# Performance work log

Hardware: AMD Instinct MI355X
Metric: run time of the kernel (lower is better)

The kernel has to match this reference:

```python
import jax, jax.numpy as jnp
import numpy as np

N, OBS, H, M, L = 512, 32, 128, 128, 3


def _w(key, shape, fan_in):
    return jax.random.normal(key, shape, dtype=jnp.float32) / np.sqrt(fan_in)


def setup_inputs() -> dict:
    key = jax.random.key(0)
    ks = iter(jax.random.split(key, 64))
    inp = {}
    inp["obs"] = jax.random.normal(next(ks), (N, OBS), dtype=jnp.float32)
    inp["pos"] = jax.random.uniform(next(ks), (N, 2), dtype=jnp.float32)
    # encoder: obs_dim -> H -> H -> H
    inp["enc_W1"] = _w(next(ks), (H, OBS), OBS); inp["enc_b1"] = jnp.zeros((H,), jnp.float32)
    inp["enc_W2"] = _w(next(ks), (H, H), H);     inp["enc_b2"] = jnp.zeros((H,), jnp.float32)
    inp["enc_W3"] = _w(next(ks), (H, H), H);     inp["enc_b3"] = jnp.zeros((H,), jnp.float32)
    # per-layer message MLPs: (2H+1) -> M -> M -> M, stacked over L layers
    inp["msg_W1"] = _w(next(ks), (L, M, 2 * H + 1), 2 * H + 1); inp["msg_b1"] = jnp.zeros((L, M), jnp.float32)
    inp["msg_W2"] = _w(next(ks), (L, M, M), M);                 inp["msg_b2"] = jnp.zeros((L, M), jnp.float32)
    inp["msg_W3"] = _w(next(ks), (L, M, M), M);                 inp["msg_b3"] = jnp.zeros((L, M), jnp.float32)
    # per-layer update MLPs: (H+M) -> H -> H -> H, stacked over L layers
    inp["upd_W1"] = _w(next(ks), (L, H, H + M), H + M); inp["upd_b1"] = jnp.zeros((L, H), jnp.float32)
    inp["upd_W2"] = _w(next(ks), (L, H, H), H);         inp["upd_b2"] = jnp.zeros((L, H), jnp.float32)
    inp["upd_W3"] = _w(next(ks), (L, H, H), H);         inp["upd_b3"] = jnp.zeros((L, H), jnp.float32)
    return inp


def _mlp3(x, W1, b1, W2, b2, W3, b3):
    h = jax.nn.relu(x @ W1.T + b1)
    h = jax.nn.relu(h @ W2.T + b2)
    return h @ W3.T + b3


def reference(obs, pos, enc_W1, enc_b1, enc_W2, enc_b2, enc_W3, enc_b3,
              msg_W1, msg_b1, msg_W2, msg_b2, msg_W3, msg_b3,
              upd_W1, upd_b1, upd_W2, upd_b2, upd_W3, upd_b3):
    n = obs.shape[0]
    h = enc_W1.shape[0]
    z = _mlp3(obs, enc_W1, enc_b1, enc_W2, enc_b2, enc_W3, enc_b3)  # (N, H)
    # pairwise distances; guard diagonal sqrt(0) for grad safety, then zero it
    diff = pos[:, None, :] - pos[None, :, :]                  # (N, N, 2)
    sq = jnp.sum(diff * diff, axis=-1)                        # (N, N)
    eye = jnp.eye(n, dtype=pos.dtype)
    dist = jnp.sqrt(jnp.where(eye > 0, 1.0, sq)) * (1.0 - eye)
    nondiag = (1.0 - eye)[:, :, None]
    n_layers = msg_W1.shape[0]
    for l in range(n_layers):
        W1 = msg_W1[l]
        Wi, Wj, wd = W1[:, :h], W1[:, h:2 * h], W1[:, 2 * h]  # split concat [z_i, z_j, d]
        A = z @ Wi.T                                          # (N, M) receiver term
        B = z @ Wj.T                                          # (N, M) sender term
        h1 = jax.nn.relu(A[:, None, :] + B[None, :, :] + dist[:, :, None] * wd + msg_b1[l])  # (N, N, M)
        h2 = jax.nn.relu(jnp.einsum('ijm,km->ijk', h1, msg_W2[l]) + msg_b2[l])
        m = jnp.einsum('ijm,km->ijk', h2, msg_W3[l]) + msg_b3[l]
        m = m * nondiag                                       # exclude j == i
        msum = jnp.sum(m, axis=1)                             # (N, M) sum over senders j
        z = _mlp3(jnp.concatenate([z, msum], axis=-1),
                  upd_W1[l], upd_b1[l], upd_W2[l], upd_b2[l], upd_W3[l], upd_b3[l])
    return z
```

## Files before the change

kernel.cpp:

```cpp
#include <hip/hip_runtime.h>

#define NA 512
#define NOBS 32
#define NH 128

typedef const float* fp32p;
typedef __attribute__((ext_vector_type(8))) short bf16x8;
typedef __attribute__((ext_vector_type(4))) float f32x4;

__device__ __forceinline__ short f2bf(float f) {
    union { float f; unsigned u; } v; v.f = f;
    unsigned r = v.u + 0x7fffu + ((v.u >> 16) & 1u);
    return (short)(r >> 16);
}

__device__ __forceinline__ bf16x8 wfrag_f4(const float* p) {
    float4 u = *(const float4*)p;
    float4 v = *(const float4*)(p + 4);
    bf16x8 f;
    f[0] = f2bf(u.x); f[1] = f2bf(u.y); f[2] = f2bf(u.z); f[3] = f2bf(u.w);
    f[4] = f2bf(v.x); f[5] = f2bf(v.y); f[6] = f2bf(v.z); f[7] = f2bf(v.w);
    return f;
}

#define HSTR 136

__global__ __launch_bounds__(512) void enc_ab_kernel(
    fp32p obs, fp32p eW1, fp32p eb1, fp32p eW2, fp32p eb2, fp32p eW3, fp32p eb3,
    fp32p mW1, float* __restrict__ z, float* __restrict__ A, float* __restrict__ B) {
    const int i = blockIdx.x;
    const int t = threadIdx.x;
    const int nn = t >> 2;
    const int ks = t & 3;

    __shared__ float xs0[NOBS];
    __shared__ float part[4 * NH];
    __shared__ float part2[4 * NH];
    __shared__ float hx[NH], hy[NH], zz[NH];

    if (t < NOBS) xs0[t] = obs[(size_t)i * NOBS + t];
    __syncthreads();
    {
        const float* wr = eW1 + (size_t)nn * NOBS + ks * 8;
        const float4 w0 = *(const float4*)wr;
        const float4 w1 = *(const float4*)(wr + 4);
        const float4 x0 = *(const float4*)&xs0[ks * 8];
        const float4 x1 = *(const float4*)&xs0[ks * 8 + 4];
        part[ks * NH + nn] = w0.x * x0.x + w0.y * x0.y + w0.z * x0.z + w0.w * x0.w +
                             w1.x * x1.x + w1.y * x1.y + w1.z * x1.z + w1.w * x1.w;
    }
    __syncthreads();
    if (t < NH)
        hx[t] = fmaxf(eb1[t] + part[t] + part[NH + t] + part[2 * NH + t] + part[3 * NH + t], 0.f);
    __syncthreads();
    {
        const float* wr = eW2 + (size_t)nn * NH + ks * 4;
        float p = 0.f;
        #pragma unroll
        for (int it = 0; it < 8; ++it) {
            const float4 wv = *(const float4*)(wr + it * 16);
            const float4 xv = *(const float4*)&hx[it * 16 + ks * 4];
            p += wv.x * xv.x + wv.y * xv.y + wv.z * xv.z + wv.w * xv.w;
        }
        part[ks * NH + nn] = p;
    }
    __syncthreads();
    if (t < NH)
        hy[t] = fmaxf(eb2[t] + part[t] + part[NH + t] + part[2 * NH + t] + part[3 * NH + t], 0.f);
    __syncthreads();
    {
        const float* wr = eW3 + (size_t)nn * NH + ks * 4;
        float p = 0.f;
        #pragma unroll
        for (int it = 0; it < 8; ++it) {
            const float4 wv = *(const float4*)(wr + it * 16);
            const float4 xv = *(const float4*)&hy[it * 16 + ks * 4];
            p += wv.x * xv.x + wv.y * xv.y + wv.z * xv.z + wv.w * xv.w;
        }
        part[ks * NH + nn] = p;
    }
    __syncthreads();
    if (t < NH) {
        const float v = eb3[t] + part[t] + part[NH + t] + part[2 * NH + t] + part[3 * NH + t];
        z[(size_t)i * NH + t] = v;
        zz[t] = v;
    }
    __syncthreads();
    {
        const float* pr = mW1 + (size_t)nn * 257;
        float pa = 0.f, pb = 0.f;
        #pragma unroll
        for (int it = 0; it < 8; ++it) {
            #pragma unroll
            for (int j = 0; j < 4; ++j) {
                const int k = it * 16 + ks * 4 + j;
                const float x = zz[k];
                pa += x * pr[k];
                pb += x * pr[NH + k];
            }
        }
        part[ks * NH + nn] = pa;
        part2[ks * NH + nn] = pb;
    }
    __syncthreads();
    if (t < NH) {
        A[(size_t)i * NH + t] = part[t] + part[NH + t] + part[2 * NH + t] + part[3 * NH + t];
        B[(size_t)i * NH + t] = part2[t] + part2[NH + t] + part2[2 * NH + t] + part2[3 * NH + t];
    }
}

__global__ __launch_bounds__(512) void msg_upd_kernel(
    const float* __restrict__ A, const float* __restrict__ B,
    fp32p pos, const float* __restrict__ zin,
    fp32p W1l, fp32p b1, fp32p W2, fp32p b2, fp32p W3, fp32p b3,
    fp32p uW1, fp32p ub1, fp32p uW2, fp32p ub2, fp32p uW3, fp32p ub3,
    fp32p msgW1n, int do_ab,
    float* __restrict__ zout, float* __restrict__ An, float* __restrict__ Bn) {
    const int i = blockIdx.x;
    const int t = threadIdx.x;
    const int lane = t & 63;
    const int w = t >> 6;
    const int q = lane >> 4;
    const int c = lane & 15;
    const int ncol = w * 16 + c;

    __shared__ short h1s[128 * HSTR];
    __shared__ short h2s[128 * HSTR];
    __shared__ float distrow[NA];
    __shared__ float amrow[NH];
    __shared__ float wdsr[NH];
    __shared__ float xs2[2 * NH];
    __shared__ float part[4 * NH];
    __shared__ float part2[4 * NH];
    __shared__ float hx[NH], hy[NH], hz[NH];

    if (t < NH) {
        amrow[t] = A[i * NH + t] + b1[t];
        wdsr[t]  = W1l[t * 257 + 256];
        xs2[t] = zin[(size_t)i * NH + t];
    }
    {
        const float2 pi = *(const float2*)&pos[2 * i];
        const float2 pj = *(const float2*)&pos[2 * t];
        const float dx = pi.x - pj.x, dy = pi.y - pj.y;
        const float s = dx * dx + dy * dy;
        distrow[t] = (t == i) ? 0.0f : sqrtf(s);
    }

    bf16x8 w2f[4], w3f[4];
    {
        const float* w2r = W2 + (size_t)ncol * NH + q * 8;
        const float* w3r = W3 + (size_t)ncol * NH + q * 8;
        #pragma unroll
        for (int kb = 0; kb < 4; ++kb) {
            w2f[kb] = wfrag_f4(w2r + kb * 32);
            w3f[kb] = wfrag_f4(w3r + kb * 32);
        }
    }
    const float b2n = b2[ncol];
    const float b3n = b3[ncol];

    const int m2 = lane * 2;
    float psum = 0.0f;

    for (int c4 = 0; c4 < 4; ++c4) {
        const int j0 = c4 * 128;
        __syncthreads();

        {
            const float am0 = amrow[m2],     am1 = amrow[m2 + 1];
            const float wd0 = wdsr[m2],      wd1 = wdsr[m2 + 1];
            #pragma unroll
            for (int rr = 0; rr < 16; ++rr) {
                const int row = rr * 8 + w;
                const int jg  = j0 + row;
                const float2 bv = *(const float2*)&B[(size_t)jg * NH + m2];
                const float d = distrow[jg];
                const float v0 = fmaxf(am0 + bv.x + d * wd0, 0.0f);
                const float v1 = fmaxf(am1 + bv.y + d * wd1, 0.0f);
                const unsigned p = (unsigned)(unsigned short)f2bf(v0) |
                                   ((unsigned)(unsigned short)f2bf(v1) << 16);
                *(unsigned*)&h1s[row * HSTR + m2] = p;
            }
        }
        __syncthreads();

        #pragma unroll
        for (int jt = 0; jt < 8; ++jt) {
            f32x4 acc = {0.f, 0.f, 0.f, 0.f};
            const short* arow = &h1s[(jt * 16 + c) * HSTR + q * 8];
            #pragma unroll
            for (int kb = 0; kb < 4; ++kb) {
                bf16x8 a = *(const bf16x8*)(arow + kb * 32);
                acc = __builtin_amdgcn_mfma_f32_16x16x32_bf16(a, w2f[kb], acc, 0, 0, 0);
            }
            #pragma unroll
            for (int r = 0; r < 4; ++r) {
                const int row = jt * 16 + q * 4 + r;
                h2s[row * HSTR + ncol] = f2bf(fmaxf(acc[r] + b2n, 0.0f));
            }
        }
        __syncthreads();

        #pragma unroll
        for (int jt = 0; jt < 8; ++jt) {
            f32x4 acc = {0.f, 0.f, 0.f, 0.f};
            const short* arow = &h2s[(jt * 16 + c) * HSTR + q * 8];
            #pragma unroll
            for (int kb = 0; kb < 4; ++kb) {
                bf16x8 a = *(const bf16x8*)(arow + kb * 32);
                acc = __builtin_amdgcn_mfma_f32_16x16x32_bf16(a, w3f[kb], acc, 0, 0, 0);
            }
            #pragma unroll
            for (int r = 0; r < 4; ++r) {
                const int jg = j0 + jt * 16 + q * 4 + r;
                if (jg != i) psum += acc[r] + b3n;
            }
        }
    }

    psum += __shfl_xor(psum, 16, 64);
    psum += __shfl_xor(psum, 32, 64);
    if (lane < 16) xs2[NH + ncol] = psum;
    __syncthreads();

    const int nn = t >> 2;
    const int ks = t & 3;
    {
        const float* wr = uW1 + (size_t)nn * 256 + ks * 4;
        float p = 0.f;
        #pragma unroll
        for (int it = 0; it < 16; ++it) {
            const float4 wv = *(const float4*)(wr + it * 16);
            const float4 xv = *(const float4*)&xs2[it * 16 + ks * 4];
            p += wv.x * xv.x + wv.y * xv.y + wv.z * xv.z + wv.w * xv.w;
        }
        part[ks * NH + nn] = p;
    }
    __syncthreads();
    if (t < NH)
        hx[t] = fmaxf(ub1[t] + part[t] + part[NH + t] + part[2 * NH + t] + part[3 * NH + t], 0.f);
    __syncthreads();
    {
        const float* wr = uW2 + (size_t)nn * NH + ks * 4;
        float p = 0.f;
        #pragma unroll
        for (int it = 0; it < 8; ++it) {
            const float4 wv = *(const float4*)(wr + it * 16);
            const float4 xv = *(const float4*)&hx[it * 16 + ks * 4];
            p += wv.x * xv.x + wv.y * xv.y + wv.z * xv.z + wv.w * xv.w;
        }
        part[ks * NH + nn] = p;
    }
    __syncthreads();
    if (t < NH)
        hy[t] = fmaxf(ub2[t] + part[t] + part[NH + t] + part[2 * NH + t] + part[3 * NH + t], 0.f);
    __syncthreads();
    {
        const float* wr = uW3 + (size_t)nn * NH + ks * 4;
        float p = 0.f;
        #pragma unroll
        for (int it = 0; it < 8; ++it) {
            const float4 wv = *(const float4*)(wr + it * 16);
            const float4 xv = *(const float4*)&hy[it * 16 + ks * 4];
            p += wv.x * xv.x + wv.y * xv.y + wv.z * xv.z + wv.w * xv.w;
        }
        part[ks * NH + nn] = p;
    }
    __syncthreads();
    if (t < NH) {
        const float v = ub3[t] + part[t] + part[NH + t] + part[2 * NH + t] + part[3 * NH + t];
        zout[(size_t)i * NH + t] = v;
        hz[t] = v;
    }
    if (!do_ab) return;
    __syncthreads();
    {
        const float* pr = msgW1n + (size_t)nn * 257;
        float pa = 0.f, pb = 0.f;
        #pragma unroll
        for (int it = 0; it < 8; ++it) {
            #pragma unroll
            for (int j = 0; j < 4; ++j) {
                const int k = it * 16 + ks * 4 + j;
                const float x = hz[k];
                pa += x * pr[k];
                pb += x * pr[NH + k];
            }
        }
        part[ks * NH + nn] = pa;
        part2[ks * NH + nn] = pb;
    }
    __syncthreads();
    if (t < NH) {
        An[(size_t)i * NH + t] = part[t] + part[NH + t] + part[2 * NH + t] + part[3 * NH + t];
        Bn[(size_t)i * NH + t] = part2[t] + part2[NH + t] + part2[2 * NH + t] + part2[3 * NH + t];
    }
}

extern "C" void kernel_launch(void* const* d_in, const int* in_sizes, int n_in,
                              void* d_out, int out_size, void* d_ws, size_t ws_size,
                              hipStream_t stream) {
    fp32p obs   = (fp32p)d_in[0];
    fp32p pos   = (fp32p)d_in[1];
    fp32p encW1 = (fp32p)d_in[2];  fp32p encb1 = (fp32p)d_in[3];
    fp32p encW2 = (fp32p)d_in[4];  fp32p encb2 = (fp32p)d_in[5];
    fp32p encW3 = (fp32p)d_in[6];  fp32p encb3 = (fp32p)d_in[7];
    fp32p msgW1 = (fp32p)d_in[8];  fp32p msgb1 = (fp32p)d_in[9];
    fp32p msgW2 = (fp32p)d_in[10]; fp32p msgb2 = (fp32p)d_in[11];
    fp32p msgW3 = (fp32p)d_in[12]; fp32p msgb3 = (fp32p)d_in[13];
    fp32p updW1 = (fp32p)d_in[14]; fp32p updb1 = (fp32p)d_in[15];
    fp32p updW2 = (fp32p)d_in[16]; fp32p updb2 = (fp32p)d_in[17];
    fp32p updW3 = (fp32p)d_in[18]; fp32p updb3 = (fp32p)d_in[19];

    float* ws = (float*)d_ws;
    float* zA = ws;
    float* zB = zA + NA * NH;
    float* A0 = zB + NA * NH;
    float* B0 = A0 + NA * NH;
    float* A1 = B0 + NA * NH;
    float* B1 = A1 + NA * NH;

    enc_ab_kernel<<<NA, 512, 0, stream>>>(obs, encW1, encb1, encW2, encb2,
                                          encW3, encb3, msgW1, zA, A0, B0);

    float* zin = zA;  float* zout = zB;
    float* Ac = A0;   float* Bc = B0;
    float* An = A1;   float* Bn = B1;
    for (int l = 0; l < 3; ++l) {
        const int do_ab = (l < 2);
        float* dst = (l == 2) ? (float*)d_out : zout;
        msg_upd_kernel<<<NA, 512, 0, stream>>>(Ac, Bc, pos, zin,
            msgW1 + (size_t)l * 128 * 257, msgb1 + l * 128,
            msgW2 + (size_t)l * 128 * 128, msgb2 + l * 128,
            msgW3 + (size_t)l * 128 * 128, msgb3 + l * 128,
            updW1 + (size_t)l * 256 * 128, updb1 + l * 128,
            updW2 + (size_t)l * 128 * 128, updb2 + l * 128,
            updW3 + (size_t)l * 128 * 128, updb3 + l * 128,
            msgW1 + (size_t)(l + 1 < 3 ? l + 1 : 0) * 128 * 257, do_ab,
            dst, An, Bn);
        float* tmp;
        tmp = zin; zin = zout; zout = tmp;
        tmp = Ac; Ac = An; An = tmp;
        tmp = Bc; Bc = Bn; Bn = tmp;
    }
}
```

Measured before the change: 227.3 us.

## Retile message MLP MFMA work, swizzle LDS, and overlap h1 build with GEMM

Each wave now computes a 64-row by 32-column tile, two accumulators sharing one A fragment, instead of 128 rows by 16 columns. This halves LDS reads of activations per MFMA. The padded LDS rows are replaced by XOR-swizzled 128-wide rows, and bf16 packing uses the hardware v_cvt_pk_bf16_f32 instruction. Building the next chunk's h1 is moved after the second GEMM so one barrier per chunk is removed, and the b3 bias is applied once as 511*b3 after the reduction. In exchange, each thread holds twice as many weight-fragment registers, under a launch_bounds hint of 4 blocks per CU.

```diff
diff --git a/kernel.cpp b/kernel.cpp
--- a/kernel.cpp
+++ b/kernel.cpp
@@ -12,6 +12,12 @@
     union { float f; unsigned u; } v; v.f = f;
     unsigned r = v.u + 0x7fffu + ((v.u >> 16) & 1u);
     return (short)(r >> 16);
+}
+
+__device__ __forceinline__ unsigned cvt_pk_bf16(float lo, float hi) {
+    unsigned r;
+    asm("v_cvt_pk_bf16_f32 %0, %1, %2" : "=v"(r) : "v"(lo), "v"(hi));
+    return r;
 }
 
 __device__ __forceinline__ bf16x8 wfrag_f4(const float* p) {
@@ -23,8 +29,6 @@
     return f;
 }
 
-#define HSTR 136
-
 __global__ __launch_bounds__(512) void enc_ab_kernel(
     fp32p obs, fp32p eW1, fp32p eb1, fp32p eW2, fp32p eb2, fp32p eW3, fp32p eb3,
     fp32p mW1, float* __restrict__ z, float* __restrict__ A, float* __restrict__ B) {
@@ -109,7 +113,7 @@
     }
 }
 
-__global__ __launch_bounds__(512) void msg_upd_kernel(
+__global__ __launch_bounds__(512, 4) void msg_upd_kernel(
     const float* __restrict__ A, const float* __restrict__ B,
     fp32p pos, const float* __restrict__ zin,
     fp32p W1l, fp32p b1, fp32p W2, fp32p b2, fp32p W3, fp32p b3,
@@ -122,10 +126,14 @@
     const int w = t >> 6;
     const int q = lane >> 4;
     const int c = lane & 15;
-    const int ncol = w * 16 + c;
-
-    __shared__ short h1s[128 * HSTR];
-    __shared__ short h2s[128 * HSTR];
+    const int q8 = q * 8;
+    const int rg = w >> 2;
+    const int cg = w & 3;
+    const int col0 = cg * 32 + c;
+    const int col1 = col0 + 16;
+
+    __shared__ short h1s[128 * 128];
+    __shared__ short h2s[128 * 128];
     __shared__ float distrow[NA];
     __shared__ float amrow[NH];
     __shared__ float wdsr[NH];
@@ -147,81 +155,109 @@
         distrow[t] = (t == i) ? 0.0f : sqrtf(s);
     }
 
-    bf16x8 w2f[4], w3f[4];
-    {
-        const float* w2r = W2 + (size_t)ncol * NH + q * 8;
-        const float* w3r = W3 + (size_t)ncol * NH + q * 8;
+    bf16x8 w2f0[4], w2f1[4], w3f0[4], w3f1[4];
+    {
+        const float* w2r0 = W2 + (size_t)col0 * NH + q8;
+        const float* w2r1 = W2 + (size_t)col1 * NH + q8;
+        const float* w3r0 = W3 + (size_t)col0 * NH + q8;
+        const float* w3r1 = W3 + (size_t)col1 * NH + q8;
         #pragma unroll
         for (int kb = 0; kb < 4; ++kb) {
-            w2f[kb] = wfrag_f4(w2r + kb * 32);
-            w3f[kb] = wfrag_f4(w3r + kb * 32);
-        }
-    }
-    const float b2n = b2[ncol];
-    const float b3n = b3[ncol];
+            w2f0[kb] = wfrag_f4(w2r0 + kb * 32);
+            w2f1[kb] = wfrag_f4(w2r1 + kb * 32);
+            w3f0[kb] = wfrag_f4(w3r0 + kb * 32);
+            w3f1[kb] = wfrag_f4(w3r1 + kb * 32);
+        }
+    }
+    const float b2n0 = b2[col0], b2n1 = b2[col1];
+
+    __syncthreads();
 
     const int m2 = lane * 2;
-    float psum = 0.0f;
+    const int mx = m2 ^ (w << 3);
+    const float am0 = amrow[m2],     am1 = amrow[m2 + 1];
+    const float wd0 = wdsr[m2],      wd1 = wdsr[m2 + 1];
+
+#define BUILD_H1(c4_) do {                                                   \
+        const int j0_ = (c4_) * 128;                                         \
+        _Pragma("unroll")                                                    \
+        for (int rr = 0; rr < 16; ++rr) {                                    \
+            const int row_ = rr * 8 + w;                                     \
+            const int jg_ = j0_ + row_;                                      \
+            const float2 bv_ = *(const float2*)&B[(size_t)jg_ * NH + m2];    \
+            const float d_ = distrow[jg_];                                   \
+            const float v0_ = fmaxf(fmaf(d_, wd0, am0 + bv_.x), 0.0f);       \
+            const float v1_ = fmaxf(fmaf(d_, wd1, am1 + bv_.y), 0.0f);       \
+            *(unsigned*)&h1s[(row_ << 7) + mx] = cvt_pk_bf16(v0_, v1_);      \
+        }                                                                    \
+    } while (0)
+
+    float psum0 = 0.0f, psum1 = 0.0f;
+
+    BUILD_H1(0);
+    __syncthreads();
 
     for (int c4 = 0; c4 < 4; ++c4) {
-        const int j0 = c4 * 128;
+        #pragma unroll
+        for (int jt = 0; jt < 4; ++jt) {
+            const int row = rg * 64 + jt * 16 + c;
+            const int rb = row << 7;
+            const int sw = (row & 7) << 3;
+            f32x4 acc0 = {0.f, 0.f, 0.f, 0.f};
+            f32x4 acc1 = {0.f, 0.f, 0.f, 0.f};
+            #pragma unroll
+            for (int kb = 0; kb < 4; ++kb) {
+                const bf16x8 a = *(const bf16x8*)&h1s[rb + ((q8 + kb * 32) ^ sw)];
+                acc0 = __builtin_amdgcn_mfma_f32_16x16x32_bf16(a, w2f0[kb], acc0, 0, 0, 0);
+                acc1 = __builtin_amdgcn_mfma_f32_16x16x32_bf16(a, w2f1[kb], acc1, 0, 0, 0);
+            }
+            #pragma unroll
+            for (int r = 0; r < 4; ++r) {
+                const int orow = rg * 64 + jt * 16 + q * 4 + r;
+                const unsigned p = cvt_pk_bf16(fmaxf(acc0[r] + b2n0, 0.0f),
+                                               fmaxf(acc1[r] + b2n1, 0.0f));
+                const int osw = (orow & 7) << 3;
+                h2s[(orow << 7) + (col0 ^ osw)] = (short)p;
+                h2s[(orow << 7) + (col1 ^ osw)] = (short)(p >> 16);
+            }
+        }
         __syncthreads();
 
-        {
-            const float am0 = amrow[m2],     am1 = amrow[m2 + 1];
-            const float wd0 = wdsr[m2],      wd1 = wdsr[m2 + 1];
-            #pragma unroll
-            for (int rr = 0; rr < 16; ++rr) {
-                const int row = rr * 8 + w;
-                const int jg  = j0 + row;
-                const float2 bv = *(const float2*)&B[(size_t)jg * NH + m2];
-                const float d = distrow[jg];
-                const float v0 = fmaxf(am0 + bv.x + d * wd0, 0.0f);
-                const float v1 = fmaxf(am1 + bv.y + d * wd1, 0.0f);
-                const unsigned p = (unsigned)(unsigned short)f2bf(v0) |
-                                   ((unsigned)(unsigned short)f2bf(v1) << 16);
-                *(unsigned*)&h1s[row * HSTR + m2] = p;
-            }
-        }
+        #pragma unroll
+        for (int jt = 0; jt < 4; ++jt) {
+            const int row = rg * 64 + jt * 16 + c;
+            const int rb = row << 7;
+            const int sw = (row & 7) << 3;
+            f32x4 acc0 = {0.f, 0.f, 0.f, 0.f};
+            f32x4 acc1 = {0.f, 0.f, 0.f, 0.f};
+            #pragma unroll
+            for (int kb = 0; kb < 4; ++kb) {
+                const bf16x8 a = *(const bf16x8*)&h2s[rb + ((q8 + kb * 32) ^ sw)];
+                acc0 = __builtin_amdgcn_mfma_f32_16x16x32_bf16(a, w3f0[kb], acc0, 0, 0, 0);
+                acc1 = __builtin_amdgcn_mfma_f32_16x16x32_bf16(a, w3f1[kb], acc1, 0, 0, 0);
+            }
+            const int jbase = c4 * 128 + rg * 64 + jt * 16 + q * 4;
+            #pragma unroll
+            for (int r = 0; r < 4; ++r) {
+                const int jg = jbase + r;
+                if (jg != i) { psum0 += acc0[r]; psum1 += acc1[r]; }
+            }
+        }
+        if (c4 < 3) BUILD_H1(c4 + 1);
         __syncthreads();
-
-        #pragma unroll
-        for (int jt = 0; jt < 8; ++jt) {
-            f32x4 acc = {0.f, 0.f, 0.f, 0.f};
-            const short* arow = &h1s[(jt * 16 + c) * HSTR + q * 8];
-            #pragma unroll
-            for (int kb = 0; kb < 4; ++kb) {
-                bf16x8 a = *(const bf16x8*)(arow + kb * 32);
-                acc = __builtin_amdgcn_mfma_f32_16x16x32_bf16(a, w2f[kb], acc, 0, 0, 0);
-            }
-            #pragma unroll
-            for (int r = 0; r < 4; ++r) {
-                const int row = jt * 16 + q * 4 + r;
-                h2s[row * HSTR + ncol] = f2bf(fmaxf(acc[r] + b2n, 0.0f));
-            }
-        }
-        __syncthreads();
-
-        #pragma unroll
-        for (int jt = 0; jt < 8; ++jt) {
-            f32x4 acc = {0.f, 0.f, 0.f, 0.f};
-            const short* arow = &h2s[(jt * 16 + c) * HSTR + q * 8];
-            #pragma unroll
-            for (int kb = 0; kb < 4; ++kb) {
-                bf16x8 a = *(const bf16x8*)(arow + kb * 32);
-                acc = __builtin_amdgcn_mfma_f32_16x16x32_bf16(a, w3f[kb], acc, 0, 0, 0);
-            }
-            #pragma unroll
-            for (int r = 0; r < 4; ++r) {
-                const int jg = j0 + jt * 16 + q * 4 + r;
-                if (jg != i) psum += acc[r] + b3n;
-            }
-        }
-    }
-
-    psum += __shfl_xor(psum, 16, 64);
-    psum += __shfl_xor(psum, 32, 64);
-    if (lane < 16) xs2[NH + ncol] = psum;
+    }
+#undef BUILD_H1
+
+    psum0 += __shfl_xor(psum0, 16, 64);
+    psum0 += __shfl_xor(psum0, 32, 64);
+    psum1 += __shfl_xor(psum1, 16, 64);
+    psum1 += __shfl_xor(psum1, 32, 64);
+    if (lane < 16) {
+        part[rg * 128 + col0] = psum0;
+        part[rg * 128 + col1] = psum1;
+    }
+    __syncthreads();
+    if (t < NH) xs2[NH + t] = part[t] + part[128 + t] + 511.0f * b3[t];
     __syncthreads();
 
     const int nn = t >> 2;
```

After: 480.0 us. 2.11x slower.
